# Optimization experiments

Measured on AMD Instinct MI355X. Metric: run time of the kernel, lower is better.

## Reference

```python
import jax, jax.numpy as jnp
import numpy as np

B, N, K = 32, 128, 16
F_ATOM, F_NEI, D = 256, 256, 256
H = 4
DK = D // H
NEG = -1e9
EPS = 1e-5
SLOPE = 0.2  # LeakyReLU slope (GAT convention)


def setup_inputs() -> dict:
    key = jax.random.key(0)
    ks = jax.random.split(key, 10)
    atom_feature = jax.random.normal(ks[0], (B, N, F_ATOM), jnp.float32)
    atom_neighbor_feature = jax.random.normal(ks[1], (B, N, K, F_NEI), jnp.float32)
    keep = (jax.random.uniform(ks[2], (B, N, K, 1)) < 0.8).astype(jnp.float32)
    atom_softmax_mask = (keep - 1.0) * (-NEG)  # 0 where valid, -1e9 where padded
    atom_attend_mask = keep
    s_a = 1.0 / np.sqrt(F_ATOM)
    s_n = 1.0 / np.sqrt(F_NEI)
    s_al = 1.0 / np.sqrt(DK)
    return {
        "atom_feature": atom_feature,
        "atom_neighbor_feature": atom_neighbor_feature,
        "atom_softmax_mask": atom_softmax_mask,
        "atom_attend_mask": atom_attend_mask,
        "W_a": jax.random.uniform(ks[3], (D, F_ATOM), jnp.float32, -s_a, s_a),
        "b_a": jnp.zeros((D,), jnp.float32),
        "W_n": jax.random.uniform(ks[4], (D, F_NEI), jnp.float32, -s_n, s_n),
        "b_n": jnp.zeros((D,), jnp.float32),
        "w_align": jax.random.uniform(ks[5], (DK,), jnp.float32, -s_al, s_al),
        "b_align": jnp.zeros((), jnp.float32),
        "ln_gamma": jnp.ones((D,), jnp.float32),
        "ln_beta": jnp.zeros((D,), jnp.float32),
    }


def reference(atom_feature, atom_neighbor_feature, atom_softmax_mask,
              atom_attend_mask, W_a, b_a, W_n, b_n, w_align, b_align,
              ln_gamma, ln_beta):
    # Linear projections (dropout is identity at inference)
    af = jnp.einsum('bnf,df->bnd', atom_feature, W_a) + b_a            # [B,N,D]
    nf = jnp.einsum('bnkf,df->bnkd', atom_neighbor_feature, W_n) + b_n  # [B,N,K,D]
    b, n, k, d = nf.shape
    afh = af.reshape(b, n, 1, H, DK)      # broadcast over neighbor axis
    nfh = nf.reshape(b, n, k, H, DK)
    # GATV2: act(Wa x_i + Wn x_j) . a
    feat = jax.nn.leaky_relu(afh + nfh, SLOPE)                          # [B,N,K,H,DK]
    score = jnp.einsum('bnkhd,d->bnkh', feat, w_align) + b_align        # [B,N,K,H]
    score = score + atom_softmax_mask                                   # [B,N,K,1] -> bcast over H
    attw = jax.nn.softmax(score, axis=2)                                # softmax over neighbors
    attw = attw * atom_attend_mask                                      # zero out padded neighbors
    ctx = jnp.einsum('bnkh,bnkhd->bnhd', attw, nfh).reshape(b, n, d)    # weighted sum
    # LayerNorm
    mu = jnp.mean(ctx, axis=-1, keepdims=True)
    var = jnp.mean(jnp.square(ctx - mu), axis=-1, keepdims=True)
    out = (ctx - mu) * jax.lax.rsqrt(var + EPS) * ln_gamma + ln_beta
    return out
```

## Files before the change

kernel.cpp:

```cpp
#include <hip/hip_runtime.h>
#include <hip/hip_bf16.h>


typedef float f32x4 __attribute__((ext_vector_type(4)));
typedef __bf16 bf16x8 __attribute__((ext_vector_type(8)));

__device__ __forceinline__ unsigned short f2bf(float x) {
    unsigned int u = __float_as_uint(x);
    u += 0x7FFFu + ((u >> 16) & 1u);
    return (unsigned short)(u >> 16);
}

__global__ __launch_bounds__(256) void conv_w(const float* __restrict__ wa,
                                              const float* __restrict__ wn,
                                              unsigned short* __restrict__ owa,
                                              unsigned short* __restrict__ own) {
    const int g = blockIdx.x * 256 + threadIdx.x;
    const float* src = (g & 8192) ? wn : wa;
    unsigned short* dst = (g & 8192) ? own : owa;
    const int c = g & 8191;
    const int lane = c & 63, ni = (c >> 6) & 3, kk = (c >> 8) & 7, wv = c >> 11;
    const int d = wv * 64 + ni * 16 + (lane & 15);
    const int f = kk * 32 + (lane >> 4) * 8;
    const float* sp = src + d * 256 + f;
    unsigned short h[8];
#pragma unroll
    for (int j = 0; j < 8; ++j) h[j] = f2bf(sp[j]);
    *(uint4*)(dst + c * 8) = *(const uint4*)h;
}

struct Smem2 {
    union {
        char  a[48 * 512];
        float nf[32][264];
    } u;
    float af[2][256];
    float wal[64];
    float attw[2][4][16];
    float red[4][2][2];
};

__global__ __launch_bounds__(256, 3) void gat_fused(
        const float* __restrict__ atomf, const float* __restrict__ nei,
        const unsigned short* __restrict__ wn_p, const unsigned short* __restrict__ wa_p,
        const float* __restrict__ b_n, const float* __restrict__ b_a,
        const float* __restrict__ smask, const float* __restrict__ amask,
        const float* __restrict__ w_align, const float* __restrict__ b_align,
        const float* __restrict__ gamma, const float* __restrict__ beta,
        float* __restrict__ out) {
    __shared__ Smem2 s;
    const int tid = threadIdx.x;
    const int p = blockIdx.x;

    if (tid < 64) s.wal[tid] = w_align[tid];

    const float4* src4 = (const float4*)(nei + (size_t)p * 32 * 256);
#pragma unroll
    for (int j = 0; j < 8; ++j) {
        const int idx4 = tid + j * 256;
        const float4 v = src4[idx4];
        const int r = idx4 >> 6;
        const int byt = (idx4 & 63) * 8;
        ushort4 h;
        h.x = f2bf(v.x); h.y = f2bf(v.y); h.z = f2bf(v.z); h.w = f2bf(v.w);
        *(ushort4*)(s.u.a + r * 512 + (byt ^ ((r & 7) << 4))) = h;
    }
    if (tid < 128) {
        const int at = tid >> 6, cc = tid & 63;
        const float4 v = *(const float4*)(atomf + (size_t)(p * 2 + at) * 256 + cc * 4);
        const int r = 32 + at;
        ushort4 h;
        h.x = f2bf(v.x); h.y = f2bf(v.y); h.z = f2bf(v.z); h.w = f2bf(v.w);
        *(ushort4*)(s.u.a + r * 512 + ((cc * 8) ^ ((r & 7) << 4))) = h;
    }
    __syncthreads();

    const int lane = tid & 63, wv = tid >> 6, l15 = lane & 15, lg = lane >> 4;

    f32x4 acc[3][4];
#pragma unroll
    for (int mi = 0; mi < 3; ++mi)
#pragma unroll
        for (int ni = 0; ni < 4; ++ni)
#pragma unroll
            for (int j = 0; j < 4; ++j) acc[mi][ni][j] = 0.f;

    const unsigned short* wn_wv = wn_p + wv * 16384 + lane * 8;
    const unsigned short* wa_wv = wa_p + wv * 16384 + lane * 8;
    bf16x8 cn[4], ca[4];
#pragma unroll
    for (int ni = 0; ni < 4; ++ni) {
        cn[ni] = *(const bf16x8*)(wn_wv + ni * 512);
        ca[ni] = *(const bf16x8*)(wa_wv + ni * 512);
    }
#pragma unroll
    for (int kk = 0; kk < 8; ++kk) {
        bf16x8 nn[4], na[4];
        if (kk < 7) {
#pragma unroll
            for (int ni = 0; ni < 4; ++ni) {
                nn[ni] = *(const bf16x8*)(wn_wv + (kk + 1) * 2048 + ni * 512);
                na[ni] = *(const bf16x8*)(wa_wv + (kk + 1) * 2048 + ni * 512);
            }
        }
        const int fb = (kk * 32 + lg * 8) * 2;
        bf16x8 afr[3];
#pragma unroll
        for (int mi = 0; mi < 3; ++mi) {
            const int r = mi * 16 + l15;
            afr[mi] = *(const bf16x8*)(s.u.a + r * 512 + (fb ^ ((r & 7) << 4)));
        }
#pragma unroll
        for (int ni = 0; ni < 4; ++ni) {
            acc[0][ni] = __builtin_amdgcn_mfma_f32_16x16x32_bf16(afr[0], cn[ni], acc[0][ni], 0, 0, 0);
            acc[1][ni] = __builtin_amdgcn_mfma_f32_16x16x32_bf16(afr[1], cn[ni], acc[1][ni], 0, 0, 0);
            acc[2][ni] = __builtin_amdgcn_mfma_f32_16x16x32_bf16(afr[2], ca[ni], acc[2][ni], 0, 0, 0);
        }
        if (kk < 7) {
#pragma unroll
            for (int ni = 0; ni < 4; ++ni) { cn[ni] = nn[ni]; ca[ni] = na[ni]; }
        }
    }
    __syncthreads();

#pragma unroll
    for (int ni = 0; ni < 4; ++ni) {
        const int d = wv * 64 + ni * 16 + l15;
        const float bnv = b_n[d], bav = b_a[d];
#pragma unroll
        for (int j = 0; j < 4; ++j) {
            s.u.nf[lg * 4 + j][d]      = acc[0][ni][j] + bnv;
            s.u.nf[16 + lg * 4 + j][d] = acc[1][ni][j] + bnv;
        }
        if (lg == 0) {
            s.af[0][d] = acc[2][ni][0] + bav;
            s.af[1][d] = acc[2][ni][1] + bav;
        }
    }
    __syncthreads();

    if (tid < 128) {
        const int a = tid >> 6, h = (tid >> 4) & 3, k = tid & 15;
        const float4* af4 = (const float4*)(&s.af[a][h * 64]);
        const float4* nf4 = (const float4*)(&s.u.nf[a * 16 + k][h * 64]);
        const float4* wl4 = (const float4*)(s.wal);
        float sc = 0.f;
#pragma unroll
        for (int i = 0; i < 16; ++i) {
            const float4 x = af4[i], y = nf4[i], w = wl4[i];
            float z0 = x.x + y.x, z1 = x.y + y.y, z2 = x.z + y.z, z3 = x.w + y.w;
            z0 = fmaxf(z0, 0.2f * z0); z1 = fmaxf(z1, 0.2f * z1);
            z2 = fmaxf(z2, 0.2f * z2); z3 = fmaxf(z3, 0.2f * z3);
            sc = fmaf(z0, w.x, sc); sc = fmaf(z1, w.y, sc);
            sc = fmaf(z2, w.z, sc); sc = fmaf(z3, w.w, sc);
        }
        sc += b_align[0] + smask[p * 32 + a * 16 + k];
        float mx = sc;
#pragma unroll
        for (int o = 1; o < 16; o <<= 1) mx = fmaxf(mx, __shfl_xor(mx, o));
        const float e = __expf(sc - mx);
        float sm = e;
#pragma unroll
        for (int o = 1; o < 16; o <<= 1) sm += __shfl_xor(sm, o);
        s.attw[a][h][k] = (e / sm) * amask[p * 32 + a * 16 + k];
    }
    __syncthreads();

    const int d = tid, hh = d >> 6;
    float c0 = 0.f, c1 = 0.f;
#pragma unroll
    for (int k = 0; k < 16; ++k) c0 = fmaf(s.attw[0][hh][k], s.u.nf[k][d], c0);
#pragma unroll
    for (int k = 0; k < 16; ++k) c1 = fmaf(s.attw[1][hh][k], s.u.nf[16 + k][d], c1);
    float sm0 = c0, sq0 = c0 * c0, sm1 = c1, sq1 = c1 * c1;
#pragma unroll
    for (int o = 1; o < 64; o <<= 1) {
        sm0 += __shfl_xor(sm0, o); sq0 += __shfl_xor(sq0, o);
        sm1 += __shfl_xor(sm1, o); sq1 += __shfl_xor(sq1, o);
    }
    if (lane == 0) {
        s.red[wv][0][0] = sm0; s.red[wv][0][1] = sq0;
        s.red[wv][1][0] = sm1; s.red[wv][1][1] = sq1;
    }
    __syncthreads();
    float ts0 = 0.f, tq0 = 0.f, ts1 = 0.f, tq1 = 0.f;
#pragma unroll
    for (int q = 0; q < 4; ++q) {
        ts0 += s.red[q][0][0]; tq0 += s.red[q][0][1];
        ts1 += s.red[q][1][0]; tq1 += s.red[q][1][1];
    }
    const float g = gamma[d], be = beta[d];
    const float mu0 = ts0 * (1.f / 256.f), mu1 = ts1 * (1.f / 256.f);
    const float v0 = fmaxf(tq0 * (1.f / 256.f) - mu0 * mu0, 0.f);
    const float v1 = fmaxf(tq1 * (1.f / 256.f) - mu1 * mu1, 0.f);
    out[(size_t)(p * 2) * 256 + d]     = (c0 - mu0) * rsqrtf(v0 + 1e-5f) * g + be;
    out[(size_t)(p * 2 + 1) * 256 + d] = (c1 - mu1) * rsqrtf(v1 + 1e-5f) * g + be;
}

extern "C" void kernel_launch(void* const* d_in, const int* in_sizes, int n_in,
                              void* d_out, int out_size, void* d_ws, size_t ws_size,
                              hipStream_t stream) {
    const float* atomf = (const float*)d_in[0];
    const float* nei   = (const float*)d_in[1];
    const float* smask = (const float*)d_in[2];
    const float* amask = (const float*)d_in[3];
    const float* Wa    = (const float*)d_in[4];
    const float* ba    = (const float*)d_in[5];
    const float* Wn    = (const float*)d_in[6];
    const float* bn    = (const float*)d_in[7];
    const float* wal   = (const float*)d_in[8];
    const float* bal   = (const float*)d_in[9];
    const float* gam   = (const float*)d_in[10];
    const float* bet   = (const float*)d_in[11];
    float* out = (float*)d_out;

    char* ws = (char*)d_ws;
    unsigned short* wa_bf = (unsigned short*)ws;
    unsigned short* wn_bf = (unsigned short*)(ws + 131072);

    hipLaunchKernelGGL(conv_w, dim3(64), dim3(256), 0, stream,
                       Wa, Wn, wa_bf, wn_bf);
    hipLaunchKernelGGL(gat_fused, dim3(2048), dim3(256), 0, stream,
                       atomf, nei, wn_bf, wa_bf, bn, ba, smask, amask,
                       wal, bal, gam, bet, out);
}
```

Before: 142.8 us.

## Split atom projection into own kernel and process four atoms per block in registers

Moves the atom-feature projection (W_a) into a separate small kernel that writes projected atom features to workspace. The main kernel now handles four atoms (64 neighbor rows) per block and computes the score, softmax, weighted context and LayerNorm statistics directly from MFMA accumulator registers with cross-lane shuffles, instead of staging the neighbor projections through LDS. This removes the LDS round trip, the 12 wasted padded rows of the atom MFMA tile and several barriers, and halves the grid. In exchange it adds an extra kernel launch, a workspace buffer round trip for af, and higher register pressure from the 16 accumulator tiles.

```diff
diff --git a/kernel.cpp b/kernel.cpp
--- a/kernel.cpp
+++ b/kernel.cpp
@@ -29,172 +29,204 @@
     *(uint4*)(dst + c * 8) = *(const uint4*)h;
 }
 
-struct Smem2 {
-    union {
-        char  a[48 * 512];
-        float nf[32][264];
-    } u;
-    float af[2][256];
+__global__ __launch_bounds__(256) void proj_atoms(const float* __restrict__ atomf,
+                                                  const unsigned short* __restrict__ wa_p,
+                                                  const float* __restrict__ b_a,
+                                                  float* __restrict__ af) {
+    __shared__ char lds[16 * 512];
+    const int tid = threadIdx.x, p = blockIdx.x;
+    const float4* src4 = (const float4*)(atomf + (size_t)p * 16 * 256);
+#pragma unroll
+    for (int j = 0; j < 4; ++j) {
+        const int idx4 = tid + j * 256;
+        const float4 v = src4[idx4];
+        const int r = idx4 >> 6, byt = (idx4 & 63) * 8;
+        ushort4 h;
+        h.x = f2bf(v.x); h.y = f2bf(v.y); h.z = f2bf(v.z); h.w = f2bf(v.w);
+        *(ushort4*)(lds + r * 512 + (byt ^ ((r & 7) << 4))) = h;
+    }
+    __syncthreads();
+    const int lane = tid & 63, wv = tid >> 6, l15 = lane & 15, lg = lane >> 4;
+    f32x4 acc[4];
+#pragma unroll
+    for (int ni = 0; ni < 4; ++ni)
+#pragma unroll
+        for (int j = 0; j < 4; ++j) acc[ni][j] = 0.f;
+    const unsigned short* w = wa_p + wv * 16384 + lane * 8;
+#pragma unroll
+    for (int kk = 0; kk < 8; ++kk) {
+        const int fb = (kk * 32 + lg * 8) * 2;
+        const int r = l15;
+        const bf16x8 afr = *(const bf16x8*)(lds + r * 512 + (fb ^ ((r & 7) << 4)));
+#pragma unroll
+        for (int ni = 0; ni < 4; ++ni) {
+            const bf16x8 cn = *(const bf16x8*)(w + kk * 2048 + ni * 512);
+            acc[ni] = __builtin_amdgcn_mfma_f32_16x16x32_bf16(afr, cn, acc[ni], 0, 0, 0);
+        }
+    }
+#pragma unroll
+    for (int ni = 0; ni < 4; ++ni) {
+        const int d = wv * 64 + ni * 16 + l15;
+        const float bav = b_a[d];
+#pragma unroll
+        for (int j = 0; j < 4; ++j)
+            af[(size_t)(p * 16 + lg * 4 + j) * 256 + d] = acc[ni][j] + bav;
+    }
+}
+
+struct SmemG {
+    char  a[64 * 512];
+    float af[4][256];
     float wal[64];
-    float attw[2][4][16];
-    float red[4][2][2];
+    float sm[4][16];
+    float am[4][16];
+    float red[4][4][2];
 };
 
-__global__ __launch_bounds__(256, 3) void gat_fused(
-        const float* __restrict__ atomf, const float* __restrict__ nei,
-        const unsigned short* __restrict__ wn_p, const unsigned short* __restrict__ wa_p,
-        const float* __restrict__ b_n, const float* __restrict__ b_a,
+__global__ __launch_bounds__(256, 4) void gat4(
+        const float* __restrict__ nei, const float* __restrict__ af_buf,
+        const unsigned short* __restrict__ wn_p, const float* __restrict__ b_n,
         const float* __restrict__ smask, const float* __restrict__ amask,
         const float* __restrict__ w_align, const float* __restrict__ b_align,
         const float* __restrict__ gamma, const float* __restrict__ beta,
         float* __restrict__ out) {
-    __shared__ Smem2 s;
+    __shared__ SmemG s;
     const int tid = threadIdx.x;
     const int p = blockIdx.x;
 
-    if (tid < 64) s.wal[tid] = w_align[tid];
-
-    const float4* src4 = (const float4*)(nei + (size_t)p * 32 * 256);
-#pragma unroll
-    for (int j = 0; j < 8; ++j) {
+    const float4* src4 = (const float4*)(nei + (size_t)p * 64 * 256);
+#pragma unroll
+    for (int j = 0; j < 16; ++j) {
         const int idx4 = tid + j * 256;
         const float4 v = src4[idx4];
-        const int r = idx4 >> 6;
-        const int byt = (idx4 & 63) * 8;
+        const int r = idx4 >> 6, byt = (idx4 & 63) * 8;
         ushort4 h;
         h.x = f2bf(v.x); h.y = f2bf(v.y); h.z = f2bf(v.z); h.w = f2bf(v.w);
-        *(ushort4*)(s.u.a + r * 512 + (byt ^ ((r & 7) << 4))) = h;
-    }
-    if (tid < 128) {
-        const int at = tid >> 6, cc = tid & 63;
-        const float4 v = *(const float4*)(atomf + (size_t)(p * 2 + at) * 256 + cc * 4);
-        const int r = 32 + at;
-        ushort4 h;
-        h.x = f2bf(v.x); h.y = f2bf(v.y); h.z = f2bf(v.z); h.w = f2bf(v.w);
-        *(ushort4*)(s.u.a + r * 512 + ((cc * 8) ^ ((r & 7) << 4))) = h;
+        *(ushort4*)(s.a + r * 512 + (byt ^ ((r & 7) << 4))) = h;
+    }
+#pragma unroll
+    for (int a2 = 0; a2 < 4; ++a2)
+        s.af[a2][tid] = af_buf[(size_t)p * 1024 + a2 * 256 + tid];
+    if (tid < 64) {
+        s.wal[tid] = w_align[tid];
+        ((float*)s.sm)[tid] = smask[p * 64 + tid];
+        ((float*)s.am)[tid] = amask[p * 64 + tid];
     }
     __syncthreads();
 
     const int lane = tid & 63, wv = tid >> 6, l15 = lane & 15, lg = lane >> 4;
 
-    f32x4 acc[3][4];
-#pragma unroll
-    for (int mi = 0; mi < 3; ++mi)
+    f32x4 acc[4][4];
+#pragma unroll
+    for (int a = 0; a < 4; ++a)
 #pragma unroll
         for (int ni = 0; ni < 4; ++ni)
 #pragma unroll
-            for (int j = 0; j < 4; ++j) acc[mi][ni][j] = 0.f;
-
-    const unsigned short* wn_wv = wn_p + wv * 16384 + lane * 8;
-    const unsigned short* wa_wv = wa_p + wv * 16384 + lane * 8;
-    bf16x8 cn[4], ca[4];
+            for (int j = 0; j < 4; ++j) acc[a][ni][j] = 0.f;
+
+    const unsigned short* w = wn_p + wv * 16384 + lane * 8;
+#pragma unroll
+    for (int kk = 0; kk < 8; ++kk) {
+        const int fb = (kk * 32 + lg * 8) * 2;
+        bf16x8 afr[4];
+#pragma unroll
+        for (int a = 0; a < 4; ++a) {
+            const int r = a * 16 + l15;
+            afr[a] = *(const bf16x8*)(s.a + r * 512 + (fb ^ ((r & 7) << 4)));
+        }
+#pragma unroll
+        for (int ni = 0; ni < 4; ++ni) {
+            const bf16x8 cn = *(const bf16x8*)(w + kk * 2048 + ni * 512);
+#pragma unroll
+            for (int a = 0; a < 4; ++a)
+                acc[a][ni] = __builtin_amdgcn_mfma_f32_16x16x32_bf16(afr[a], cn, acc[a][ni], 0, 0, 0);
+        }
+    }
+
+    float bn4[4], wl4[4];
 #pragma unroll
     for (int ni = 0; ni < 4; ++ni) {
-        cn[ni] = *(const bf16x8*)(wn_wv + ni * 512);
-        ca[ni] = *(const bf16x8*)(wa_wv + ni * 512);
-    }
-#pragma unroll
-    for (int kk = 0; kk < 8; ++kk) {
-        bf16x8 nn[4], na[4];
-        if (kk < 7) {
+        bn4[ni] = b_n[wv * 64 + ni * 16 + l15];
+        wl4[ni] = s.wal[ni * 16 + l15];
+    }
+#pragma unroll
+    for (int a = 0; a < 4; ++a)
+#pragma unroll
+        for (int ni = 0; ni < 4; ++ni)
+#pragma unroll
+            for (int j = 0; j < 4; ++j) acc[a][ni][j] += bn4[ni];
+
+    const float bal = b_align[0];
+    float ctx[4][4];
+#pragma unroll
+    for (int a = 0; a < 4; ++a) {
+        float afd[4];
+#pragma unroll
+        for (int ni = 0; ni < 4; ++ni)
+            afd[ni] = s.af[a][wv * 64 + ni * 16 + l15];
+        float sj[4];
+#pragma unroll
+        for (int j = 0; j < 4; ++j) {
+            float t = 0.f;
 #pragma unroll
             for (int ni = 0; ni < 4; ++ni) {
-                nn[ni] = *(const bf16x8*)(wn_wv + (kk + 1) * 2048 + ni * 512);
-                na[ni] = *(const bf16x8*)(wa_wv + (kk + 1) * 2048 + ni * 512);
+                float z = afd[ni] + acc[a][ni][j];
+                z = fmaxf(z, 0.2f * z);
+                t = fmaf(z, wl4[ni], t);
             }
-        }
-        const int fb = (kk * 32 + lg * 8) * 2;
-        bf16x8 afr[3];
-#pragma unroll
-        for (int mi = 0; mi < 3; ++mi) {
-            const int r = mi * 16 + l15;
-            afr[mi] = *(const bf16x8*)(s.u.a + r * 512 + (fb ^ ((r & 7) << 4)));
-        }
+            sj[j] = t;
+        }
+#pragma unroll
+        for (int j = 0; j < 4; ++j) {
+#pragma unroll
+            for (int o = 1; o < 16; o <<= 1) sj[j] += __shfl_xor(sj[j], o);
+            sj[j] += bal + s.sm[a][lg * 4 + j];
+        }
+        float m = fmaxf(fmaxf(sj[0], sj[1]), fmaxf(sj[2], sj[3]));
+        m = fmaxf(m, __shfl_xor(m, 16));
+        m = fmaxf(m, __shfl_xor(m, 32));
+        float e[4], sum = 0.f;
+#pragma unroll
+        for (int j = 0; j < 4; ++j) { e[j] = __expf(sj[j] - m); sum += e[j]; }
+        sum += __shfl_xor(sum, 16);
+        sum += __shfl_xor(sum, 32);
+        const float inv = 1.f / sum;
+        float aw[4];
+#pragma unroll
+        for (int j = 0; j < 4; ++j) aw[j] = e[j] * inv * s.am[a][lg * 4 + j];
 #pragma unroll
         for (int ni = 0; ni < 4; ++ni) {
-            acc[0][ni] = __builtin_amdgcn_mfma_f32_16x16x32_bf16(afr[0], cn[ni], acc[0][ni], 0, 0, 0);
-            acc[1][ni] = __builtin_amdgcn_mfma_f32_16x16x32_bf16(afr[1], cn[ni], acc[1][ni], 0, 0, 0);
-            acc[2][ni] = __builtin_amdgcn_mfma_f32_16x16x32_bf16(afr[2], ca[ni], acc[2][ni], 0, 0, 0);
-        }
-        if (kk < 7) {
-#pragma unroll
-            for (int ni = 0; ni < 4; ++ni) { cn[ni] = nn[ni]; ca[ni] = na[ni]; }
-        }
+            float c = 0.f;
+#pragma unroll
+            for (int j = 0; j < 4; ++j) c = fmaf(aw[j], acc[a][ni][j], c);
+            c += __shfl_xor(c, 16);
+            c += __shfl_xor(c, 32);
+            ctx[a][ni] = c;
+        }
+        float t = 0.f, q = 0.f;
+#pragma unroll
+        for (int ni = 0; ni < 4; ++ni) { t += ctx[a][ni]; q = fmaf(ctx[a][ni], ctx[a][ni], q); }
+#pragma unroll
+        for (int o = 1; o < 16; o <<= 1) { t += __shfl_xor(t, o); q += __shfl_xor(q, o); }
+        if (lane == 0) { s.red[wv][a][0] = t; s.red[wv][a][1] = q; }
     }
     __syncthreads();
 
-#pragma unroll
-    for (int ni = 0; ni < 4; ++ni) {
-        const int d = wv * 64 + ni * 16 + l15;
-        const float bnv = b_n[d], bav = b_a[d];
-#pragma unroll
-        for (int j = 0; j < 4; ++j) {
-            s.u.nf[lg * 4 + j][d]      = acc[0][ni][j] + bnv;
-            s.u.nf[16 + lg * 4 + j][d] = acc[1][ni][j] + bnv;
-        }
-        if (lg == 0) {
-            s.af[0][d] = acc[2][ni][0] + bav;
-            s.af[1][d] = acc[2][ni][1] + bav;
-        }
-    }
-    __syncthreads();
-
-    if (tid < 128) {
-        const int a = tid >> 6, h = (tid >> 4) & 3, k = tid & 15;
-        const float4* af4 = (const float4*)(&s.af[a][h * 64]);
-        const float4* nf4 = (const float4*)(&s.u.nf[a * 16 + k][h * 64]);
-        const float4* wl4 = (const float4*)(s.wal);
-        float sc = 0.f;
-#pragma unroll
-        for (int i = 0; i < 16; ++i) {
-            const float4 x = af4[i], y = nf4[i], w = wl4[i];
-            float z0 = x.x + y.x, z1 = x.y + y.y, z2 = x.z + y.z, z3 = x.w + y.w;
-            z0 = fmaxf(z0, 0.2f * z0); z1 = fmaxf(z1, 0.2f * z1);
-            z2 = fmaxf(z2, 0.2f * z2); z3 = fmaxf(z3, 0.2f * z3);
-            sc = fmaf(z0, w.x, sc); sc = fmaf(z1, w.y, sc);
-            sc = fmaf(z2, w.z, sc); sc = fmaf(z3, w.w, sc);
-        }
-        sc += b_align[0] + smask[p * 32 + a * 16 + k];
-        float mx = sc;
-#pragma unroll
-        for (int o = 1; o < 16; o <<= 1) mx = fmaxf(mx, __shfl_xor(mx, o));
-        const float e = __expf(sc - mx);
-        float sm = e;
-#pragma unroll
-        for (int o = 1; o < 16; o <<= 1) sm += __shfl_xor(sm, o);
-        s.attw[a][h][k] = (e / sm) * amask[p * 32 + a * 16 + k];
-    }
-    __syncthreads();
-
-    const int d = tid, hh = d >> 6;
-    float c0 = 0.f, c1 = 0.f;
-#pragma unroll
-    for (int k = 0; k < 16; ++k) c0 = fmaf(s.attw[0][hh][k], s.u.nf[k][d], c0);
-#pragma unroll
-    for (int k = 0; k < 16; ++k) c1 = fmaf(s.attw[1][hh][k], s.u.nf[16 + k][d], c1);
-    float sm0 = c0, sq0 = c0 * c0, sm1 = c1, sq1 = c1 * c1;
-#pragma unroll
-    for (int o = 1; o < 64; o <<= 1) {
-        sm0 += __shfl_xor(sm0, o); sq0 += __shfl_xor(sq0, o);
-        sm1 += __shfl_xor(sm1, o); sq1 += __shfl_xor(sq1, o);
-    }
-    if (lane == 0) {
-        s.red[wv][0][0] = sm0; s.red[wv][0][1] = sq0;
-        s.red[wv][1][0] = sm1; s.red[wv][1][1] = sq1;
-    }
-    __syncthreads();
-    float ts0 = 0.f, tq0 = 0.f, ts1 = 0.f, tq1 = 0.f;
-#pragma unroll
-    for (int q = 0; q < 4; ++q) {
-        ts0 += s.red[q][0][0]; tq0 += s.red[q][0][1];
-        ts1 += s.red[q][1][0]; tq1 += s.red[q][1][1];
-    }
-    const float g = gamma[d], be = beta[d];
-    const float mu0 = ts0 * (1.f / 256.f), mu1 = ts1 * (1.f / 256.f);
-    const float v0 = fmaxf(tq0 * (1.f / 256.f) - mu0 * mu0, 0.f);
-    const float v1 = fmaxf(tq1 * (1.f / 256.f) - mu1 * mu1, 0.f);
-    out[(size_t)(p * 2) * 256 + d]     = (c0 - mu0) * rsqrtf(v0 + 1e-5f) * g + be;
-    out[(size_t)(p * 2 + 1) * 256 + d] = (c1 - mu1) * rsqrtf(v1 + 1e-5f) * g + be;
+    const float g = gamma[wv * 64 + lane];
+    const float be = beta[wv * 64 + lane];
+#pragma unroll
+    for (int a = 0; a < 4; ++a) {
+        float ts = 0.f, tq = 0.f;
+#pragma unroll
+        for (int q2 = 0; q2 < 4; ++q2) { ts += s.red[q2][a][0]; tq += s.red[q2][a][1]; }
+        const float mu = ts * (1.f / 256.f);
+        float var = tq * (1.f / 256.f) - mu * mu;
+        var = fmaxf(var, 0.f);
+        const float rs = rsqrtf(var + 1e-5f);
+        const float cv = (lg == 0) ? ctx[a][0] : (lg == 1) ? ctx[a][1]
+                        : (lg == 2) ? ctx[a][2] : ctx[a][3];
+        out[(size_t)(p * 4 + a) * 256 + wv * 64 + lane] = (cv - mu) * rs * g + be;
+    }
 }
 
 extern "C" void kernel_launch(void* const* d_in, const int* in_sizes, int n_in,
@@ -215,12 +247,15 @@
     float* out = (float*)d_out;
 
     char* ws = (char*)d_ws;
-    unsigned short* wa_bf = (unsigned short*)ws;
-    unsigned short* wn_bf = (unsigned short*)(ws + 131072);
+    float*          af_buf = (float*)ws;
+    unsigned short* wa_bf  = (unsigned short*)(ws + 4194304);
+    unsigned short* wn_bf  = (unsigned short*)(ws + 4194304 + 131072);
 
     hipLaunchKernelGGL(conv_w, dim3(64), dim3(256), 0, stream,
                        Wa, Wn, wa_bf, wn_bf);
-    hipLaunchKernelGGL(gat_fused, dim3(2048), dim3(256), 0, stream,
-                       atomf, nei, wn_bf, wa_bf, bn, ba, smask, amask,
+    hipLaunchKernelGGL(proj_atoms, dim3(256), dim3(256), 0, stream,
+                       atomf, wa_bf, ba, af_buf);
+    hipLaunchKernelGGL(gat4, dim3(1024), dim3(256), 0, stream,
+                       nei, af_buf, wn_bf, bn, smask, amask,
                        wal, bal, gam, bet, out);
 }
```

Result: faster. 136.5 us (-4.4%).
